# Optimization experiments

Measured on AMD Instinct MI355X. Metric: run time of the kernel, lower is better.

## Reference

```python
import jax, jax.numpy as jnp
import numpy as np

B, O, E, H = 8192, 256, 64, 4  # batch, num_orbital, num_electron, hidden size


def setup_inputs() -> dict:
    key = jax.random.key(0)
    kx, k1, k2, k3, k4, k5, k6 = jax.random.split(key, 7)
    # occupancy vector: exactly E ones per sample among O orbitals
    perm_keys = jax.random.split(kx, B)
    occ = jax.vmap(lambda k: jax.random.permutation(k, O)[:E])(perm_keys)  # [B, E]
    x = jnp.zeros((B, O), jnp.float32).at[jnp.arange(B)[:, None], occ].set(1.0)
    # hidden Dense layers (kernel_init = uniform[0, 0.2), bias = zeros, as in flax default bias)
    W1 = jax.random.uniform(k1, (O, H), jnp.float32, 0.0, 0.2)
    b1 = jnp.zeros((H,), jnp.float32)
    W2 = jax.random.uniform(k2, (H, H), jnp.float32, 0.0, 0.2)
    b2 = jnp.zeros((H,), jnp.float32)
    # DenseGeneral: H -> (O, E); lecun_normal-ish init
    Wg = jax.random.normal(k3, (H, O, E), jnp.float32) / jnp.sqrt(jnp.float32(H))
    bg = jnp.zeros((O, E), jnp.float32)
    return {"x": x, "W1": W1, "b1": b1, "W2": W2, "b2": b2, "Wg": Wg, "bg": bg}


def reference(x, W1, b1, W2, b2, Wg, bg):
    # occupied orbital indices, ascending, fixed size E (vmapped jnp.nonzero)
    sel = jax.vmap(lambda row: jnp.nonzero(row, size=E, fill_value=0)[0])(x)  # [B, E] int
    # tiny MLP
    h = jax.nn.relu(x @ W1 + b1)        # [B, H]
    h = jax.nn.relu(h @ W2 + b2)        # [B, H]
    # DenseGeneral projection: [B, H] x [H, O, E] -> [B, O, E]
    M = jnp.einsum('bh,hoe->boe', h, Wg) + bg
    # gather occupied rows -> [B, E, E]
    rows = jnp.take_along_axis(M, sel[:, :, None], axis=1)
    return jnp.linalg.det(rows)          # [B]
```

## Files before the change

kernel.cpp:

```cpp
#include <hip/hip_runtime.h>

#define BB 8192
#define OO 256
#define EE 64
#define HH 4

__device__ __forceinline__ float rlanef(float v, int lane) {
    return __int_as_float(__builtin_amdgcn_readlane(__float_as_int(v), lane));
}

__global__ __launch_bounds__(256) void backflow_det_reg(
    const float* __restrict__ x,  const float* __restrict__ W1,
    const float* __restrict__ b1, const float* __restrict__ W2,
    const float* __restrict__ b2, const float* __restrict__ Wg,
    const float* __restrict__ bg, float* __restrict__ out)
{
    __shared__ int sel_lds[4][EE];

    const int tid = threadIdx.x;
    const int tx  = tid & 63;
    const int w   = tid >> 6;
    const int b   = blockIdx.x * 4 + w;

    const float* xb = x + (size_t)b * OO;
    int base = 0;
    #pragma unroll
    for (int g = 0; g < 4; ++g) {
        const float xv = xb[g * 64 + tx];
        const unsigned long long m = __ballot(xv != 0.0f);
        if (xv != 0.0f) {
            const int pos = base + __popcll(m & ((1ull << tx) - 1ull));
            sel_lds[w][pos] = g * 64 + tx;
        }
        base += __popcll(m);
    }
    const int v_sel = sel_lds[w][tx];

    const float4 w1r = *reinterpret_cast<const float4*>(W1 + v_sel * HH);
    float s0 = w1r.x, s1 = w1r.y, s2 = w1r.z, s3 = w1r.w;
    #pragma unroll
    for (int d = 32; d >= 1; d >>= 1) {
        s0 += __shfl_xor(s0, d);
        s1 += __shfl_xor(s1, d);
        s2 += __shfl_xor(s2, d);
        s3 += __shfl_xor(s3, d);
    }
    const float h0 = fmaxf(s0 + b1[0], 0.0f);
    const float h1 = fmaxf(s1 + b1[1], 0.0f);
    const float h2 = fmaxf(s2 + b1[2], 0.0f);
    const float h3 = fmaxf(s3 + b1[3], 0.0f);
    float c[HH];
    #pragma unroll
    for (int j = 0; j < HH; ++j) {
        float t = b2[j];
        t = fmaf(h0, W2[0 * HH + j], t);
        t = fmaf(h1, W2[1 * HH + j], t);
        t = fmaf(h2, W2[2 * HH + j], t);
        t = fmaf(h3, W2[3 * HH + j], t);
        c[j] = fmaxf(t, 0.0f);
    }

    float a[EE];
    #pragma unroll
    for (int i = 0; i < EE; ++i) {
        const int si = __builtin_amdgcn_readlane(v_sel, i);
        float t = bg[si * EE + tx];
        t = fmaf(c[0], Wg[(0 * OO + si) * EE + tx], t);
        t = fmaf(c[1], Wg[(1 * OO + si) * EE + tx], t);
        t = fmaf(c[2], Wg[(2 * OO + si) * EE + tx], t);
        t = fmaf(c[3], Wg[(3 * OO + si) * EE + tx], t);
        a[i] = t;
    }

    float l2 = 0.0f;
    unsigned int sbits = 0u;
    #pragma unroll
    for (int k = 0; k < EE; ++k) {
        const float pv  = rlanef(a[k], k);
        const float pvc = copysignf(fmaxf(fabsf(pv), 1e-20f), pv);
        sbits ^= (__float_as_uint(pvc) & 0x80000000u);
        l2 += __log2f(fabsf(pvc));
        const float ninv = -__builtin_amdgcn_rcpf(pvc);
        a[k] *= ninv;
        #pragma unroll
        for (int i = k + 1; i < EE; ++i) {
            const float m = rlanef(a[i], k);
            a[i] = fmaf(m, a[k], a[i]);
        }
    }
    if (tx == 0) {
        const float mag = exp2f(fminf(l2, 126.0f));
        out[b] = __uint_as_float(__float_as_uint(mag) ^ sbits);
    }
}

extern "C" void kernel_launch(void* const* d_in, const int* in_sizes, int n_in,
                              void* d_out, int out_size, void* d_ws, size_t ws_size,
                              hipStream_t stream) {
    const float* x  = (const float*)d_in[0];
    const float* W1 = (const float*)d_in[1];
    const float* b1 = (const float*)d_in[2];
    const float* W2 = (const float*)d_in[3];
    const float* b2 = (const float*)d_in[4];
    const float* Wg = (const float*)d_in[5];
    const float* bg = (const float*)d_in[6];
    float* out = (float*)d_out;

    backflow_det_reg<<<dim3(BB / 4), dim3(256), 0, stream>>>(x, W1, b1, W2, b2, Wg, bg, out);
}
```

Baseline: 155.8 us.

## Broadcast pivot row through LDS with float4 reads instead of per-element readlane

Gaussian elimination previously fetched each multiplier with a scalar readlane, one per matrix entry per step, which serialises through the scalar unit. Now the pivot lane writes its remaining column to shared memory and every lane reads it back as float4 vectors for the rank-1 update. The log2-based determinant accumulation is also replaced by a running double-precision product. This adds an LDS write and read round trip per step plus implicit wave-level ordering assumptions, and the double multiply adds FP64 work in the loop.

```diff
diff --git a/kernel.cpp b/kernel.cpp
--- a/kernel.cpp
+++ b/kernel.cpp
@@ -5,8 +5,8 @@
 #define EE 64
 #define HH 4
 
-__device__ __forceinline__ float rlanef(float v, int lane) {
-    return __int_as_float(__builtin_amdgcn_readlane(__float_as_int(v), lane));
+__device__ __forceinline__ float f4get(const float4& v, int e) {
+    return e == 0 ? v.x : e == 1 ? v.y : e == 2 ? v.z : v.w;
 }
 
 __global__ __launch_bounds__(256) void backflow_det_reg(
@@ -15,7 +15,8 @@
     const float* __restrict__ b2, const float* __restrict__ Wg,
     const float* __restrict__ bg, float* __restrict__ out)
 {
-    __shared__ int sel_lds[4][EE];
+    __shared__ float mcol[4][EE];
+    __shared__ int   sel_lds[4][EE];
 
     const int tid = threadIdx.x;
     const int tx  = tid & 63;
@@ -60,37 +61,58 @@
         c[j] = fmaxf(t, 0.0f);
     }
 
-    float a[EE];
+    float4 a4[16];
     #pragma unroll
-    for (int i = 0; i < EE; ++i) {
-        const int si = __builtin_amdgcn_readlane(v_sel, i);
-        float t = bg[si * EE + tx];
-        t = fmaf(c[0], Wg[(0 * OO + si) * EE + tx], t);
-        t = fmaf(c[1], Wg[(1 * OO + si) * EE + tx], t);
-        t = fmaf(c[2], Wg[(2 * OO + si) * EE + tx], t);
-        t = fmaf(c[3], Wg[(3 * OO + si) * EE + tx], t);
-        a[i] = t;
+    for (int q = 0; q < 16; ++q) {
+        float e[4];
+        #pragma unroll
+        for (int r = 0; r < 4; ++r) {
+            const int i  = q * 4 + r;
+            const int si = __builtin_amdgcn_readlane(v_sel, i);
+            float t = bg[si * EE + tx];
+            t = fmaf(c[0], Wg[(0 * OO + si) * EE + tx], t);
+            t = fmaf(c[1], Wg[(1 * OO + si) * EE + tx], t);
+            t = fmaf(c[2], Wg[(2 * OO + si) * EE + tx], t);
+            t = fmaf(c[3], Wg[(3 * OO + si) * EE + tx], t);
+            e[r] = t;
+        }
+        a4[q] = make_float4(e[0], e[1], e[2], e[3]);
     }
 
-    float l2 = 0.0f;
-    unsigned int sbits = 0u;
+    float*  mb  = &mcol[w][0];
+    float4* mb4 = reinterpret_cast<float4*>(mb);
+    double det_d = 1.0;
     #pragma unroll
     for (int k = 0; k < EE; ++k) {
-        const float pv  = rlanef(a[k], k);
-        const float pvc = copysignf(fmaxf(fabsf(pv), 1e-20f), pv);
-        sbits ^= (__float_as_uint(pvc) & 0x80000000u);
-        l2 += __log2f(fabsf(pvc));
+        const int t0 = k >> 2;
+        if (tx == k) {
+            #pragma unroll
+            for (int t = t0; t < 16; ++t) mb4[t] = a4[t];
+        }
+        const float4 c0  = mb4[t0];
+        const float  pv  = f4get(c0, k & 3);
+        const float  pvc = copysignf(fmaxf(fabsf(pv), 1e-20f), pv);
+        det_d *= (double)pvc;
         const float ninv = -__builtin_amdgcn_rcpf(pvc);
-        a[k] *= ninv;
+        const float u_   = f4get(a4[t0], k & 3) * ninv;
+        a4[t0].x = fmaf(c0.x, u_, a4[t0].x);
+        a4[t0].y = fmaf(c0.y, u_, a4[t0].y);
+        a4[t0].z = fmaf(c0.z, u_, a4[t0].z);
+        a4[t0].w = fmaf(c0.w, u_, a4[t0].w);
         #pragma unroll
-        for (int i = k + 1; i < EE; ++i) {
-            const float m = rlanef(a[i], k);
-            a[i] = fmaf(m, a[k], a[i]);
+        for (int t = t0 + 1; t < 16; ++t) {
+            const float4 mv = mb4[t];
+            a4[t].x = fmaf(mv.x, u_, a4[t].x);
+            a4[t].y = fmaf(mv.y, u_, a4[t].y);
+            a4[t].z = fmaf(mv.z, u_, a4[t].z);
+            a4[t].w = fmaf(mv.w, u_, a4[t].w);
         }
     }
     if (tx == 0) {
-        const float mag = exp2f(fminf(l2, 126.0f));
-        out[b] = __uint_as_float(__float_as_uint(mag) ^ sbits);
+        double dd = det_d;
+        dd = fmin(dd, 3.0e38);
+        dd = fmax(dd, -3.0e38);
+        out[b] = (float)dd;
     }
 }
 
```

Result: slower. 201.3 us (+29.2%).
